# Performance work log

Measured on AMD Instinct MI355X. Metric: run time of the kernel, lower is better.

The kernel has to match this reference:

```python
import jax, jax.numpy as jnp
import numpy as np

B, T, E, HD, K, V = 128, 512, 128, 128, 20, 30000  # HD = hidden per direction


def _lstm_dir(x, Wih, Whh, b, reverse):
    # x: [T, B, D]; Wih: [4H, D]; Whh: [4H, H]; b: [4H] (b_ih + b_hh combined)
    if reverse:
        x = x[::-1]
    bsz = x.shape[1]
    xW = jnp.einsum('tbd,gd->tbg', x, Wih) + b  # [T, B, 4H] precompute input proj
    h0 = jnp.zeros((bsz, HD), x.dtype)
    c0 = jnp.zeros((bsz, HD), x.dtype)

    def step(carry, xw):
        h, c = carry
        z = xw + h @ Whh.T
        i, f, g, o = jnp.split(z, 4, axis=-1)  # PyTorch gate order i,f,g,o
        c = jax.nn.sigmoid(f) * c + jax.nn.sigmoid(i) * jnp.tanh(g)
        h = jax.nn.sigmoid(o) * jnp.tanh(c)
        return (h, c), h

    _, hs = jax.lax.scan(step, (h0, c0), xW)
    if reverse:
        hs = hs[::-1]
    return hs


def _bilstm_layer(x, Wih, Whh, b):
    # Wih/Whh: [2, 4H, D]/[2, 4H, H]; b: [2, 4H]
    hf = _lstm_dir(x, Wih[0], Whh[0], b[0], False)
    hb = _lstm_dir(x, Wih[1], Whh[1], b[1], True)
    return jnp.concatenate([hf, hb], axis=-1)  # [T, B, 2H]


def _crf_nll(emissions, tags, trans, start, end):
    # emissions: [B, T, K]; tags: [B, T]; full (all-ones) mask, reduction='mean'
    bsz = emissions.shape[0]
    em_tm = jnp.swapaxes(emissions, 0, 1)  # [T, B, K]
    tags_tm = tags.T                       # [T, B]
    bidx = jnp.arange(bsz)

    # --- numerator: path score ---
    score0 = start[tags_tm[0]] + em_tm[0][bidx, tags_tm[0]]

    def num_step(s, inp):
        em_t, tg_prev, tg_t = inp
        return s + trans[tg_prev, tg_t] + em_t[bidx, tg_t], None

    score, _ = jax.lax.scan(num_step, score0, (em_tm[1:], tags_tm[:-1], tags_tm[1:]))
    score = score + end[tags_tm[-1]]

    # --- denominator: forward algorithm (log partition) ---
    alpha0 = start[None, :] + em_tm[0]  # [B, K]

    def den_step(a, em_t):
        # a[b,i] + trans[i,j] + em_t[b,j] -> logsumexp over i
        a = jax.nn.logsumexp(a[:, :, None] + trans[None], axis=1) + em_t
        return a, None

    alpha, _ = jax.lax.scan(den_step, alpha0, em_tm[1:])
    logZ = jax.nn.logsumexp(alpha + end[None, :], axis=1)

    return -jnp.mean(score - logZ)


def setup_inputs() -> dict:
    key = jax.random.key(0)
    ks = jax.random.split(key, 16)
    u = lambda k, shape, s: jax.random.uniform(k, shape, jnp.float32, -s, s)
    kk = 1.0 / np.sqrt(HD)
    embed = jax.random.normal(ks[0], (V, E), jnp.float32) * 0.1
    embed = embed.at[0].set(0.0)  # padding_idx=0
    inp = {
        'sentences': jax.random.randint(ks[1], (B, T), 1, V),  # no pad tokens -> full mask
        'tags': jax.random.randint(ks[2], (B, T), 0, K),
        'lengths': jnp.full((B,), T, dtype=jnp.int64 if jax.config.jax_enable_x64 else jnp.int32),
        'embed': embed,
        'Wih0': u(ks[3], (2, 4 * HD, E), kk),
        'Whh0': u(ks[4], (2, 4 * HD, HD), kk),
        'b0': u(ks[5], (2, 4 * HD), kk),
        'Wih1': u(ks[6], (2, 4 * HD, 2 * HD), kk),
        'Whh1': u(ks[7], (2, 4 * HD, HD), kk),
        'b1': u(ks[8], (2, 4 * HD), kk),
        'Wout': u(ks[9], (K, 2 * HD), 1.0 / np.sqrt(2 * HD)),
        'bout': u(ks[10], (K,), 1.0 / np.sqrt(2 * HD)),
        'trans': u(ks[11], (K, K), 0.1),
        'start': u(ks[12], (K,), 0.1),
        'end': u(ks[13], (K,), 0.1),
    }
    return inp


def reference(sentences, tags, lengths, embed, Wih0, Whh0, b0, Wih1, Whh1, b1, Wout, bout, trans, start, end):
    # all lengths == T, so pack/pad is identity (eval-mode: no dropout)
    x = embed[sentences]                 # [B, T, E]
    x = jnp.swapaxes(x, 0, 1)            # [T, B, E] time-major for scan
    x = _bilstm_layer(x, Wih0, Whh0, b0)  # [T, B, 2H]
    x = _bilstm_layer(x, Wih1, Whh1, b1)  # [T, B, 2H]
    emissions = jnp.einsum('tbh,kh->tbk', x, Wout) + bout  # [T, B, K]
    emissions = jnp.swapaxes(emissions, 0, 1)              # [B, T, K]
    return _crf_nll(emissions, tags, trans, start, end)
```

## Files before the change

kernel.cpp:

```cpp
#include <hip/hip_runtime.h>
#include <hip/hip_bf16.h>
#include <cstddef>

typedef unsigned short u16;
typedef short bf16x8 __attribute__((ext_vector_type(8)));
typedef unsigned short u16x8 __attribute__((ext_vector_type(8)));
typedef float f32x4 __attribute__((ext_vector_type(4)));

constexpr int CB = 128;
constexpr int CT = 512;
constexpr int CE = 128;
constexpr int CK = 20;

constexpr size_t OFF_FLAG  = 0;
constexpr size_t OFF_WIH0  = 256;
constexpr size_t OFF_WHH0  = OFF_WIH0 + 262144;
constexpr size_t OFF_WIH1  = OFF_WHH0 + 262144;
constexpr size_t OFF_WHH1  = OFF_WIH1 + 524288;
constexpr size_t OFF_WOUT  = OFF_WHH1 + 262144;
constexpr size_t OFF_B0    = OFF_WOUT + 10240;
constexpr size_t OFF_B1    = OFF_B0 + 4096;
constexpr size_t OFF_BOUT  = OFF_B1 + 4096;
constexpr size_t OFF_TRANS = OFF_BOUT + 256;
constexpr size_t OFF_START = OFF_TRANS + 1792;
constexpr size_t OFF_END   = OFF_START + 256;
constexpr size_t OFF_PART  = OFF_END + 256;
constexpr size_t OFF_X0    = 2097152;
constexpr size_t OFF_H0    = OFF_X0 + 16777216;
constexpr size_t OFF_H1    = OFF_H0 + 33554432;
constexpr size_t OFF_EM    = OFF_H1 + 33554432;
constexpr size_t OFF_Z     = OFF_EM + 5242880;
constexpr size_t WS_NEED   = OFF_Z + 134217728;

__device__ __forceinline__ float b2f(u16 u) {
    union { unsigned int i; float f; } v; v.i = ((unsigned int)u) << 16; return v.f;
}
__device__ __forceinline__ u16 f2b(float f) {
    union { float f; unsigned int i; } v; v.f = f;
    unsigned int r = v.i + 0x7FFFu + ((v.i >> 16) & 1u);
    return (u16)(r >> 16);
}
__device__ __forceinline__ float ldin(const void* p, long i, int bf) {
    return bf ? b2f(((const u16*)p)[i]) : ((const float*)p)[i];
}
__device__ __forceinline__ float sigm(float x) { return 1.0f / (1.0f + __expf(-x)); }
__device__ __forceinline__ float tanh_f(float x) { return 2.0f / (1.0f + __expf(-2.0f * x)) - 1.0f; }

__global__ void sniff_k(const unsigned char* __restrict__ traw, int* __restrict__ flag) {
    int lane = threadIdx.x;
    int votes = 0;
    for (int w = lane; w < 200; w += 64) {
        unsigned char b1 = traw[w * 4 + 1];
        unsigned char e = b1 & 0x7F;
        if (e >= 0x20 && e <= 0x3E) votes++;
    }
    #pragma unroll
    for (int off = 32; off; off >>= 1) votes += __shfl_xor(votes, off);
    if (lane == 0) *flag = (votes > 120) ? 1 : 0;
}

__global__ __launch_bounds__(256) void prep_k(
    const void* wih0, const void* whh0, const void* b0,
    const void* wih1, const void* whh1, const void* b1,
    const void* wout, const void* bout, const void* trans,
    const void* start, const void* end, unsigned char* ws)
{
    const int bf = *(const int*)(ws + OFF_FLAG);
    long tid = (long)blockIdx.x * 256 + threadIdx.x;
    u16* wih0b = (u16*)(ws + OFF_WIH0);
    u16* whh0b = (u16*)(ws + OFF_WHH0);
    u16* wih1b = (u16*)(ws + OFF_WIH1);
    u16* whh1b = (u16*)(ws + OFF_WHH1);
    u16* woutb = (u16*)(ws + OFF_WOUT);
    float* b0f   = (float*)(ws + OFF_B0);
    float* b1f   = (float*)(ws + OFF_B1);
    float* boutf = (float*)(ws + OFF_BOUT);
    float* trf   = (float*)(ws + OFF_TRANS);
    float* stf   = (float*)(ws + OFF_START);
    float* enf   = (float*)(ws + OFF_END);

    if (tid < 131072) { wih0b[tid] = f2b(ldin(wih0, tid, bf)); return; } tid -= 131072;
    if (tid < 131072) { whh0b[tid] = f2b(ldin(whh0, tid, bf)); return; } tid -= 131072;
    if (tid < 1024)   { b0f[tid]   = ldin(b0, tid, bf);        return; } tid -= 1024;
    if (tid < 262144) { wih1b[tid] = f2b(ldin(wih1, tid, bf)); return; } tid -= 262144;
    if (tid < 131072) { whh1b[tid] = f2b(ldin(whh1, tid, bf)); return; } tid -= 131072;
    if (tid < 1024)   { b1f[tid]   = ldin(b1, tid, bf);        return; } tid -= 1024;
    if (tid < 5120)   { woutb[tid] = f2b(ldin(wout, tid, bf)); return; } tid -= 5120;
    if (tid < 20)     { boutf[tid] = ldin(bout, tid, bf);      return; } tid -= 20;
    if (tid < 400)    { trf[tid]   = ldin(trans, tid, bf);     return; } tid -= 400;
    if (tid < 20)     { stf[tid]   = ldin(start, tid, bf);     return; } tid -= 20;
    if (tid < 20)     { enf[tid]   = ldin(end, tid, bf);       return; }
}

__global__ __launch_bounds__(256) void gather_k(const void* __restrict__ embed,
                                                const int* __restrict__ sent,
                                                unsigned char* __restrict__ ws)
{
    const int bf = *(const int*)(ws + OFF_FLAG);
    u16* x0 = (u16*)(ws + OFF_X0);
    int tid = blockIdx.x * 256 + threadIdx.x;
    int m = tid >> 4, ch = tid & 15;
    int t = m >> 7, b = m & 127;
    int s = sent[b * CT + t];
    long src = (long)s * CE + ch * 8;
    u16x8 o;
    if (bf) {
        o = *(const u16x8*)((const u16*)embed + src);
    } else {
        const float* ef = (const float*)embed + src;
        f32x4 lo = *(const f32x4*)ef;
        f32x4 hi = *(const f32x4*)(ef + 4);
        o[0]=f2b(lo[0]); o[1]=f2b(lo[1]); o[2]=f2b(lo[2]); o[3]=f2b(lo[3]);
        o[4]=f2b(hi[0]); o[5]=f2b(hi[1]); o[6]=f2b(hi[2]); o[7]=f2b(hi[3]);
    }
    *(u16x8*)(x0 + (long)m * CE + ch * 8) = o;
}

template<int KD>
__global__ __launch_bounds__(256) void gemm_k(const u16* __restrict__ A,
                                              const u16* __restrict__ Bw,
                                              u16* __restrict__ Zp)
{
    const int bm = blockIdx.x >> 3, bn = blockIdx.x & 7;
    const long m0 = (long)bm * 128;
    const int n0 = bn * 128;
    const int tid = threadIdx.x, lane = tid & 63, wave = tid >> 6;
    const int wm = wave >> 1, wn = wave & 1;
    const int lr = lane & 15, kg = (lane >> 4) * 8;

    __shared__ __align__(16) u16 At[128][32];
    __shared__ __align__(16) u16 Bt[128][32];
    __shared__ __align__(16) u16 cho[128][136];

    f32x4 acc[4][4];
    #pragma unroll
    for (int i = 0; i < 4; ++i)
        #pragma unroll
        for (int j = 0; j < 4; ++j) acc[i][j] = (f32x4){0.f, 0.f, 0.f, 0.f};

    const int srow = tid >> 2, scol = (tid & 3) * 8;
    for (int kk = 0; kk < KD; kk += 32) {
        const u16x8 a0 = *(const u16x8*)(A + (m0 + srow) * KD + kk + scol);
        const u16x8 a1 = *(const u16x8*)(A + (m0 + srow + 64) * KD + kk + scol);
        const u16x8 b0 = *(const u16x8*)(Bw + (long)(n0 + srow) * KD + kk + scol);
        const u16x8 b1 = *(const u16x8*)(Bw + (long)(n0 + srow + 64) * KD + kk + scol);
        __syncthreads();
        *(u16x8*)&At[srow][scol] = a0;
        *(u16x8*)&At[srow + 64][scol] = a1;
        *(u16x8*)&Bt[srow][scol] = b0;
        *(u16x8*)&Bt[srow + 64][scol] = b1;
        __syncthreads();
        bf16x8 af[4], bfv[4];
        #pragma unroll
        for (int mt = 0; mt < 4; ++mt)
            af[mt] = *(const bf16x8*)&At[wm * 64 + mt * 16 + lr][kg];
        #pragma unroll
        for (int nt = 0; nt < 4; ++nt)
            bfv[nt] = *(const bf16x8*)&Bt[wn * 64 + nt * 16 + lr][kg];
        #pragma unroll
        for (int mt = 0; mt < 4; ++mt)
            #pragma unroll
            for (int nt = 0; nt < 4; ++nt)
                acc[mt][nt] = __builtin_amdgcn_mfma_f32_16x16x32_bf16(
                    af[mt], bfv[nt], acc[mt][nt], 0, 0, 0);
    }

    __syncthreads();
    const int rr0 = (lane >> 4) * 4;
    #pragma unroll
    for (int mt = 0; mt < 4; ++mt)
        #pragma unroll
        for (int nt = 0; nt < 4; ++nt) {
            const int colw = wn * 64 + nt * 16 + lr;
            const int pc = (colw & 15) * 8 + (colw >> 4);
            #pragma unroll
            for (int r = 0; r < 4; ++r)
                cho[wm * 64 + mt * 16 + rr0 + r][pc] = f2b(acc[mt][nt][r]);
        }
    __syncthreads();
    const int brow = tid >> 1, hf = tid & 1;
    const int dd = n0 >> 9, gt = (n0 >> 7) & 3;
    const int t = bm;
    const int sz = dd ? (CT - 1 - t) : t;
    u16* dst = Zp + ((long)(brow * 2 + dd) * CT + sz) * 512 + gt * 128 + hf * 64;
    const u16* srcl = &cho[brow][hf * 64];
    #pragma unroll
    for (int p = 0; p < 8; ++p)
        *(u16x8*)(dst + p * 8) = *(const u16x8*)(srcl + p * 8);
}

__global__ __launch_bounds__(256, 1) void scan_k(const u16* __restrict__ Zp,
                                                 const u16* __restrict__ Whh,
                                                 const float* __restrict__ bias,
                                                 u16* __restrict__ hout)
{
    const int b = blockIdx.x & 127, d = blockIdx.x >> 7;
    const int tid = threadIdx.x;
    const int lane = tid & 63;
    const int wave = tid >> 6;
    const int lr = lane & 15, kg = (lane >> 4) * 8;
    const int uhalf = (lane >> 4) & 1;
    const int rowm = wave * 32 + (lane & 31);

    bf16x8 bfrag[4][2][4];
    #pragma unroll
    for (int gt = 0; gt < 4; ++gt)
        #pragma unroll
        for (int uu = 0; uu < 2; ++uu) {
            const u16* wb = Whh + (long)(d * 512 + gt * 128 + wave * 32 + uu * 16 + lr) * 128 + kg;
            #pragma unroll
            for (int kt = 0; kt < 4; ++kt)
                bfrag[gt][uu][kt] = *(const bf16x8*)(wb + kt * 32);
        }
    float bgv[4];
    #pragma unroll
    for (int gt = 0; gt < 4; ++gt) bgv[gt] = bias[d * 512 + gt * 128 + rowm];

    __shared__ __align__(16) u16 hbufF[2 * 128];
    __shared__ __align__(16) u16 zbufF[2 * 8192];

    const u16* zseq = Zp + (long)(b * 2 + d) * CT * 512;
    const u16* zg = zseq + tid * 8 + 2 * 8192;

    #pragma unroll
    for (int c = 0; c < 4; ++c) {
        u16x8 v = *(const u16x8*)(zseq + tid * 8 + c * 2048);
        *(u16x8*)(zbufF + tid * 8 + c * 2048) = v;
    }
    u16x8 zr0 = *(const u16x8*)(zseq + 8192 + tid * 8);
    u16x8 zr1 = *(const u16x8*)(zseq + 8192 + tid * 8 + 2048);
    u16x8 zr2 = *(const u16x8*)(zseq + 8192 + tid * 8 + 4096);
    u16x8 zr3 = *(const u16x8*)(zseq + 8192 + tid * 8 + 6144);
    if (tid < 128) hbufF[tid] = 0;
    asm volatile("s_waitcnt lgkmcnt(0)\n\ts_barrier" ::: "memory");

    float cst = 0.f;
    u16* hp = hout + ((long)(d ? (CT - 1) : 0) * CB + b) * 256 + d * 128 + rowm;
    const long hstep = (long)(d ? -1 : 1) * CB * 256;
    const int zwi = lr * 4 + wave;

    for (int grp = 0; grp < 32; ++grp) {
        const unsigned int* zw = (const unsigned int*)(zbufF + (grp & 1) * 8192);
        u16* zbn = zbufF + ((grp + 1) & 1) * 8192;
        const bool pre = (grp >= 1) && (grp < 31);
        const bool commit = (grp < 31);
        #pragma unroll
        for (int slot = 0; slot < 16; ++slot) {
            if (slot == 0 && pre) {
                zr0 = *(const u16x8*)(zg);
                zr1 = *(const u16x8*)(zg + 2048);
                zr2 = *(const u16x8*)(zg + 4096);
                zr3 = *(const u16x8*)(zg + 6144);
            }
            unsigned int zvw[4];
            #pragma unroll
            for (int gt = 0; gt < 4; ++gt)
                zvw[gt] = zw[slot * 256 + gt * 64 + zwi];
            const u16* hbp = hbufF + (slot & 1) * 128 + kg;
            const bf16x8 av0 = *(const bf16x8*)(hbp);
            const bf16x8 av1 = *(const bf16x8*)(hbp + 32);
            const bf16x8 av2 = *(const bf16x8*)(hbp + 64);
            const bf16x8 av3 = *(const bf16x8*)(hbp + 96);

            f32x4 acc[4][2];
            #pragma unroll
            for (int gt = 0; gt < 4; ++gt) {
                acc[gt][0] = (f32x4){0.f, 0.f, 0.f, 0.f};
                acc[gt][1] = (f32x4){0.f, 0.f, 0.f, 0.f};
            }
            #pragma unroll
            for (int gt = 0; gt < 4; ++gt) {
                acc[gt][0] = __builtin_amdgcn_mfma_f32_16x16x32_bf16(av0, bfrag[gt][0][0], acc[gt][0], 0, 0, 0);
                acc[gt][1] = __builtin_amdgcn_mfma_f32_16x16x32_bf16(av0, bfrag[gt][1][0], acc[gt][1], 0, 0, 0);
            }
            #pragma unroll
            for (int gt = 0; gt < 4; ++gt) {
                acc[gt][0] = __builtin_amdgcn_mfma_f32_16x16x32_bf16(av1, bfrag[gt][0][1], acc[gt][0], 0, 0, 0);
                acc[gt][1] = __builtin_amdgcn_mfma_f32_16x16x32_bf16(av1, bfrag[gt][1][1], acc[gt][1], 0, 0, 0);
            }
            #pragma unroll
            for (int gt = 0; gt < 4; ++gt) {
                acc[gt][0] = __builtin_amdgcn_mfma_f32_16x16x32_bf16(av2, bfrag[gt][0][2], acc[gt][0], 0, 0, 0);
                acc[gt][1] = __builtin_amdgcn_mfma_f32_16x16x32_bf16(av2, bfrag[gt][1][2], acc[gt][1], 0, 0, 0);
            }
            #pragma unroll
            for (int gt = 0; gt < 4; ++gt) {
                acc[gt][0] = __builtin_amdgcn_mfma_f32_16x16x32_bf16(av3, bfrag[gt][0][3], acc[gt][0], 0, 0, 0);
                acc[gt][1] = __builtin_amdgcn_mfma_f32_16x16x32_bf16(av3, bfrag[gt][1][3], acc[gt][1], 0, 0, 0);
            }

            float pg[4];
            #pragma unroll
            for (int gt = 0; gt < 4; ++gt) {
                const float sv = uhalf ? acc[gt][1][0] : acc[gt][0][0];
                union { unsigned int i; float f; } zz;
                zz.i = uhalf ? (zvw[gt] & 0xFFFF0000u) : (zvw[gt] << 16);
                pg[gt] = sv + zz.f + bgv[gt];
            }
            const float iv = sigm(pg[0]);
            const float fv = sigm(pg[1]);
            const float gg = tanh_f(pg[2]);
            const float ov = sigm(pg[3]);
            cst = fmaf(fv, cst, iv * gg);
            const float h = ov * tanh_f(cst);

            if (slot == 15 && commit) {
                *(u16x8*)(zbn + tid * 8) = zr0;
                *(u16x8*)(zbn + tid * 8 + 2048) = zr1;
                *(u16x8*)(zbn + tid * 8 + 4096) = zr2;
                *(u16x8*)(zbn + tid * 8 + 6144) = zr3;
            }
            if (lane < 32) {
                const u16 hv = f2b(h);
                hbufF[((slot + 1) & 1) * 128 + rowm] = hv;
                *hp = hv;
            }
            hp += hstep;
            asm volatile("s_waitcnt lgkmcnt(0)\n\ts_barrier" ::: "memory");
        }
        zg += 8192;
    }
}

__global__ __launch_bounds__(256) void emis_k(const u16* __restrict__ h1,
                                              const u16* __restrict__ woutb,
                                              const float* __restrict__ boutf,
                                              float* __restrict__ em)
{
    __shared__ __align__(16) float wsm[CK * 256];
    for (int i = threadIdx.x; i < CK * 256; i += 256) wsm[i] = b2f(woutb[i]);
    __syncthreads();
    const long m = (long)blockIdx.x * 256 + threadIdx.x;
    const u16* hrow = h1 + m * 256;
    float acc[CK];
    #pragma unroll
    for (int n = 0; n < CK; ++n) acc[n] = boutf[n];
    for (int k8 = 0; k8 < 32; ++k8) {
        u16x8 u = *(const u16x8*)(hrow + k8 * 8);
        float hv[8];
        #pragma unroll
        for (int j = 0; j < 8; ++j) hv[j] = b2f(u[j]);
        #pragma unroll
        for (int n = 0; n < CK; ++n) {
            const f32x4 w0 = *(const f32x4*)&wsm[n * 256 + k8 * 8];
            const f32x4 w1 = *(const f32x4*)&wsm[n * 256 + k8 * 8 + 4];
            acc[n] = fmaf(hv[0], w0[0], acc[n]); acc[n] = fmaf(hv[1], w0[1], acc[n]);
            acc[n] = fmaf(hv[2], w0[2], acc[n]); acc[n] = fmaf(hv[3], w0[3], acc[n]);
            acc[n] = fmaf(hv[4], w1[0], acc[n]); acc[n] = fmaf(hv[5], w1[1], acc[n]);
            acc[n] = fmaf(hv[6], w1[2], acc[n]); acc[n] = fmaf(hv[7], w1[3], acc[n]);
        }
    }
    float* emrow = em + m * CK;
    #pragma unroll
    for (int n = 0; n < CK; ++n) emrow[n] = acc[n];
}

__global__ void crf_k(const float* __restrict__ em, const int* __restrict__ tags,
                      const float* __restrict__ trf, const float* __restrict__ stf,
                      const float* __restrict__ enf, float* __restrict__ partial)
{
    const int lane = threadIdx.x;
    if (blockIdx.x < 64) {
        const int j = lane & 31, half = lane >> 5;
        const int b = blockIdx.x * 2 + half;
        const bool act = j < CK;
        float tcol[CK];
        #pragma unroll
        for (int i = 0; i < CK; ++i) tcol[i] = act ? trf[i * CK + j] : 0.f;
        float alpha = act ? (stf[j] + em[(long)b * CK + j]) : 0.f;
        for (int t = 1; t < CT; ++t) {
            const float mx = __shfl(alpha, 0, 32);
            float e[CK];
            #pragma unroll
            for (int i = 0; i < CK; ++i)
                e[i] = __expf(__shfl(alpha, i, 32) - mx + tcol[i]);
            float s1[10], s2[5];
            #pragma unroll
            for (int i = 0; i < 10; ++i) s1[i] = e[2 * i] + e[2 * i + 1];
            #pragma unroll
            for (int i = 0; i < 5; ++i) s2[i] = s1[2 * i] + s1[2 * i + 1];
            const float s = (s2[0] + s2[1]) + (s2[2] + s2[3]) + s2[4];
            const float emv = act ? em[((long)t * CB + b) * CK + j] : 0.f;
            const float na = mx + __logf(s) + emv;
            alpha = act ? na : 0.f;
        }
        float vv = act ? (alpha + enf[j]) : -1e30f;
        float mx = vv;
        #pragma unroll
        for (int off = 16; off; off >>= 1) mx = fmaxf(mx, __shfl_xor(mx, off, 32));
        float ex = act ? __expf(vv - mx) : 0.f;
        #pragma unroll
        for (int off = 16; off; off >>= 1) ex += __shfl_xor(ex, off, 32);
        if (j == 0) partial[b] = mx + __logf(ex);
    } else {
        const int b = blockIdx.x - 64;
        float sc = 0.f;
        for (int t = lane; t < CT; t += 64) {
            const int tg = tags[b * CT + t];
            sc += em[((long)t * CB + b) * CK + tg];
            if (t >= 1) sc += trf[tags[b * CT + t - 1] * CK + tg];
        }
        #pragma unroll
        for (int off = 32; off; off >>= 1) sc += __shfl_xor(sc, off);
        if (lane == 0)
            partial[128 + b] = sc + stf[tags[b * CT]] + enf[tags[b * CT + CT - 1]];
    }
}

__global__ void fin_k(const float* __restrict__ partial, void* __restrict__ out,
                      const unsigned char* __restrict__ ws)
{
    const int bf = *(const int*)(ws + OFF_FLAG);
    const int lane = threadIdx.x;
    float v = (partial[lane] - partial[128 + lane]) + (partial[lane + 64] - partial[192 + lane]);
    #pragma unroll
    for (int off = 32; off; off >>= 1) v += __shfl_xor(v, off);
    if (lane == 0) {
        const float mean = v / 128.f;
        if (bf) ((u16*)out)[0] = f2b(mean);
        else    ((float*)out)[0] = mean;
    }
}

extern "C" void kernel_launch(void* const* d_in, const int* in_sizes, int n_in,
                              void* d_out, int out_size, void* d_ws, size_t ws_size,
                              hipStream_t stream) {
    (void)in_sizes; (void)n_in; (void)out_size;
    if (ws_size < WS_NEED) return;
    unsigned char* ws = (unsigned char*)d_ws;

    const void* sent  = d_in[0];
    const void* tags  = d_in[1];
    const void* embed = d_in[3];

    u16* x0  = (u16*)(ws + OFF_X0);
    u16* h0  = (u16*)(ws + OFF_H0);
    u16* h1  = (u16*)(ws + OFF_H1);
    u16* Zb  = (u16*)(ws + OFF_Z);
    float* em = (float*)(ws + OFF_EM);
    float* part = (float*)(ws + OFF_PART);

    sniff_k<<<1, 64, 0, stream>>>((const unsigned char*)d_in[12], (int*)(ws + OFF_FLAG));
    prep_k<<<2590, 256, 0, stream>>>(d_in[4], d_in[5], d_in[6], d_in[7], d_in[8],
                                     d_in[9], d_in[10], d_in[11], d_in[12], d_in[13],
                                     d_in[14], ws);
    gather_k<<<4096, 256, 0, stream>>>(embed, (const int*)sent, ws);
    gemm_k<128><<<4096, 256, 0, stream>>>(x0, (const u16*)(ws + OFF_WIH0), Zb);
    scan_k<<<256, 256, 0, stream>>>(Zb, (const u16*)(ws + OFF_WHH0),
                                    (const float*)(ws + OFF_B0), h0);
    gemm_k<256><<<4096, 256, 0, stream>>>(h0, (const u16*)(ws + OFF_WIH1), Zb);
    scan_k<<<256, 256, 0, stream>>>(Zb, (const u16*)(ws + OFF_WHH1),
                                    (const float*)(ws + OFF_B1), h1);
    emis_k<<<256, 256, 0, stream>>>(h1, (const u16*)(ws + OFF_WOUT),
                                    (const float*)(ws + OFF_BOUT), em);
    crf_k<<<192, 64, 0, stream>>>(em, (const int*)tags,
                                  (const float*)(ws + OFF_TRANS),
                                  (const float*)(ws + OFF_START),
                                  (const float*)(ws + OFF_END), part);
    fin_k<<<1, 64, 0, stream>>>(part, d_out, ws);
}
```

Before: 1.051 ms.

## Fold LSTM bias into input GEMM and stream gate inputs via registers

The input-projection GEMM now adds the gate bias in its epilogue and writes gate pre-activations in a layout where each lane's two hidden units sit in one 32-bit word. The recurrent scan kernel drops its shared-memory double buffer for gate inputs. Each lane instead keeps a 16-step register window and prefetches the next group's values per slot with direct global loads. This removes shared-memory staging and a bias add from the serial critical path. In exchange it uses many more registers and issues small scattered global loads, which could stall the latency-bound recurrence.

```diff
diff --git a/kernel.cpp b/kernel.cpp
--- a/kernel.cpp
+++ b/kernel.cpp
@@ -3,6 +3,7 @@
 #include <cstddef>
 
 typedef unsigned short u16;
+typedef unsigned int u32;
 typedef short bf16x8 __attribute__((ext_vector_type(8)));
 typedef unsigned short u16x8 __attribute__((ext_vector_type(8)));
 typedef float f32x4 __attribute__((ext_vector_type(4)));
@@ -33,11 +34,11 @@
 constexpr size_t WS_NEED   = OFF_Z + 134217728;
 
 __device__ __forceinline__ float b2f(u16 u) {
-    union { unsigned int i; float f; } v; v.i = ((unsigned int)u) << 16; return v.f;
+    union { u32 i; float f; } v; v.i = ((u32)u) << 16; return v.f;
 }
 __device__ __forceinline__ u16 f2b(float f) {
-    union { float f; unsigned int i; } v; v.f = f;
-    unsigned int r = v.i + 0x7FFFu + ((v.i >> 16) & 1u);
+    union { float f; u32 i; } v; v.f = f;
+    u32 r = v.i + 0x7FFFu + ((v.i >> 16) & 1u);
     return (u16)(r >> 16);
 }
 __device__ __forceinline__ float ldin(const void* p, long i, int bf) {
@@ -119,6 +120,7 @@
 template<int KD>
 __global__ __launch_bounds__(256) void gemm_k(const u16* __restrict__ A,
                                               const u16* __restrict__ Bw,
+                                              const float* __restrict__ bias,
                                               u16* __restrict__ Zp)
 {
     const int bm = blockIdx.x >> 3, bn = blockIdx.x & 7;
@@ -131,6 +133,8 @@
     __shared__ __align__(16) u16 At[128][32];
     __shared__ __align__(16) u16 Bt[128][32];
     __shared__ __align__(16) u16 cho[128][136];
+    __shared__ float bsm[128];
+    if (tid < 128) bsm[tid] = bias[n0 + tid];
 
     f32x4 acc[4][4];
     #pragma unroll
@@ -172,10 +176,11 @@
         #pragma unroll
         for (int nt = 0; nt < 4; ++nt) {
             const int colw = wn * 64 + nt * 16 + lr;
-            const int pc = (colw & 15) * 8 + (colw >> 4);
+            const int pc = (colw >> 5) * 32 + ((colw & 15) << 1) + ((colw >> 4) & 1);
+            const float bv = bsm[colw];
             #pragma unroll
             for (int r = 0; r < 4; ++r)
-                cho[wm * 64 + mt * 16 + rr0 + r][pc] = f2b(acc[mt][nt][r]);
+                cho[wm * 64 + mt * 16 + rr0 + r][pc] = f2b(acc[mt][nt][r] + bv);
         }
     __syncthreads();
     const int brow = tid >> 1, hf = tid & 1;
@@ -191,7 +196,6 @@
 
 __global__ __launch_bounds__(256, 1) void scan_k(const u16* __restrict__ Zp,
                                                  const u16* __restrict__ Whh,
-                                                 const float* __restrict__ bias,
                                                  u16* __restrict__ hout)
 {
     const int b = blockIdx.x & 127, d = blockIdx.x >> 7;
@@ -212,50 +216,41 @@
             for (int kt = 0; kt < 4; ++kt)
                 bfrag[gt][uu][kt] = *(const bf16x8*)(wb + kt * 32);
         }
-    float bgv[4];
-    #pragma unroll
-    for (int gt = 0; gt < 4; ++gt) bgv[gt] = bias[d * 512 + gt * 128 + rowm];
 
     __shared__ __align__(16) u16 hbufF[2 * 128];
-    __shared__ __align__(16) u16 zbufF[2 * 8192];
 
     const u16* zseq = Zp + (long)(b * 2 + d) * CT * 512;
-    const u16* zg = zseq + tid * 8 + 2 * 8192;
-
-    #pragma unroll
-    for (int c = 0; c < 4; ++c) {
-        u16x8 v = *(const u16x8*)(zseq + tid * 8 + c * 2048);
-        *(u16x8*)(zbufF + tid * 8 + c * 2048) = v;
-    }
-    u16x8 zr0 = *(const u16x8*)(zseq + 8192 + tid * 8);
-    u16x8 zr1 = *(const u16x8*)(zseq + 8192 + tid * 8 + 2048);
-    u16x8 zr2 = *(const u16x8*)(zseq + 8192 + tid * 8 + 4096);
-    u16x8 zr3 = *(const u16x8*)(zseq + 8192 + tid * 8 + 6144);
+    const u32* zw0 = (const u32*)zseq + wave * 16 + lr;
+
+    u32 zR[16][4];
+    #pragma unroll
+    for (int s = 0; s < 16; ++s) {
+        #pragma unroll
+        for (int g = 0; g < 4; ++g)
+            zR[s][g] = zw0[s * 256 + g * 64];
+    }
+    const u32* znext = zw0 + 16 * 256;
+
     if (tid < 128) hbufF[tid] = 0;
     asm volatile("s_waitcnt lgkmcnt(0)\n\ts_barrier" ::: "memory");
 
     float cst = 0.f;
     u16* hp = hout + ((long)(d ? (CT - 1) : 0) * CB + b) * 256 + d * 128 + rowm;
-    const long hstep = (long)(d ? -1 : 1) * CB * 256;
-    const int zwi = lr * 4 + wave;
+    const long hstep = (long)(d ? -1 : 1) * (CB * 256);
 
     for (int grp = 0; grp < 32; ++grp) {
-        const unsigned int* zw = (const unsigned int*)(zbufF + (grp & 1) * 8192);
-        u16* zbn = zbufF + ((grp + 1) & 1) * 8192;
-        const bool pre = (grp >= 1) && (grp < 31);
-        const bool commit = (grp < 31);
+        const bool more = grp < 31;
         #pragma unroll
         for (int slot = 0; slot < 16; ++slot) {
-            if (slot == 0 && pre) {
-                zr0 = *(const u16x8*)(zg);
-                zr1 = *(const u16x8*)(zg + 2048);
-                zr2 = *(const u16x8*)(zg + 4096);
-                zr3 = *(const u16x8*)(zg + 6144);
-            }
-            unsigned int zvw[4];
-            #pragma unroll
-            for (int gt = 0; gt < 4; ++gt)
-                zvw[gt] = zw[slot * 256 + gt * 64 + zwi];
+            const u32 zl0 = zR[slot][0], zl1 = zR[slot][1];
+            const u32 zl2 = zR[slot][2], zl3 = zR[slot][3];
+            if (more) {
+                zR[slot][0] = znext[slot * 256];
+                zR[slot][1] = znext[slot * 256 + 64];
+                zR[slot][2] = znext[slot * 256 + 128];
+                zR[slot][3] = znext[slot * 256 + 192];
+            }
+
             const u16* hbp = hbufF + (slot & 1) * 128 + kg;
             const bf16x8 av0 = *(const bf16x8*)(hbp);
             const bf16x8 av1 = *(const bf16x8*)(hbp + 32);
@@ -289,13 +284,14 @@
                 acc[gt][1] = __builtin_amdgcn_mfma_f32_16x16x32_bf16(av3, bfrag[gt][1][3], acc[gt][1], 0, 0, 0);
             }
 
+            const u32 zlw[4] = {zl0, zl1, zl2, zl3};
             float pg[4];
             #pragma unroll
             for (int gt = 0; gt < 4; ++gt) {
+                union { u32 i; float f; } zz;
+                zz.i = uhalf ? (zlw[gt] & 0xFFFF0000u) : (zlw[gt] << 16);
                 const float sv = uhalf ? acc[gt][1][0] : acc[gt][0][0];
-                union { unsigned int i; float f; } zz;
-                zz.i = uhalf ? (zvw[gt] & 0xFFFF0000u) : (zvw[gt] << 16);
-                pg[gt] = sv + zz.f + bgv[gt];
+                pg[gt] = sv + zz.f;
             }
             const float iv = sigm(pg[0]);
             const float fv = sigm(pg[1]);
@@ -304,12 +300,6 @@
             cst = fmaf(fv, cst, iv * gg);
             const float h = ov * tanh_f(cst);
 
-            if (slot == 15 && commit) {
-                *(u16x8*)(zbn + tid * 8) = zr0;
-                *(u16x8*)(zbn + tid * 8 + 2048) = zr1;
-                *(u16x8*)(zbn + tid * 8 + 4096) = zr2;
-                *(u16x8*)(zbn + tid * 8 + 6144) = zr3;
-            }
             if (lane < 32) {
                 const u16 hv = f2b(h);
                 hbufF[((slot + 1) & 1) * 128 + rowm] = hv;
@@ -318,7 +308,7 @@
             hp += hstep;
             asm volatile("s_waitcnt lgkmcnt(0)\n\ts_barrier" ::: "memory");
         }
-        zg += 8192;
+        znext += 4096;
     }
 }
 
@@ -445,12 +435,12 @@
                                      d_in[9], d_in[10], d_in[11], d_in[12], d_in[13],
                                      d_in[14], ws);
     gather_k<<<4096, 256, 0, stream>>>(embed, (const int*)sent, ws);
-    gemm_k<128><<<4096, 256, 0, stream>>>(x0, (const u16*)(ws + OFF_WIH0), Zb);
-    scan_k<<<256, 256, 0, stream>>>(Zb, (const u16*)(ws + OFF_WHH0),
-                                    (const float*)(ws + OFF_B0), h0);
-    gemm_k<256><<<4096, 256, 0, stream>>>(h0, (const u16*)(ws + OFF_WIH1), Zb);
-    scan_k<<<256, 256, 0, stream>>>(Zb, (const u16*)(ws + OFF_WHH1),
-                                    (const float*)(ws + OFF_B1), h1);
+    gemm_k<128><<<4096, 256, 0, stream>>>(x0, (const u16*)(ws + OFF_WIH0),
+                                          (const float*)(ws + OFF_B0), Zb);
+    scan_k<<<256, 256, 0, stream>>>(Zb, (const u16*)(ws + OFF_WHH0), h0);
+    gemm_k<256><<<4096, 256, 0, stream>>>(h0, (const u16*)(ws + OFF_WIH1),
+                                          (const float*)(ws + OFF_B1), Zb);
+    scan_k<<<256, 256, 0, stream>>>(Zb, (const u16*)(ws + OFF_WHH1), h1);
     emis_k<<<256, 256, 0, stream>>>(h1, (const u16*)(ws + OFF_WOUT),
                                     (const float*)(ws + OFF_BOUT), em);
     crf_k<<<192, 64, 0, stream>>>(em, (const int*)tags,
```

Result: slower. 1.085 ms (+3.2%).
